# Performance work log

Measured on AMD Instinct MI355X. Metric: run time of the kernel, lower is better.

## Reference

```python
import jax, jax.numpy as jnp
import numpy as np

BIOSYNTHETIC_FAMILIES = {'glutamate': ['E','Q','P','R','K'], 'aspartate': ['D','N','T','I','M','K'], 'serine': ['S','G','C'], 'pyruvate': ['A','V','L'], 'aromatic': ['F','Y','W'], 'histidine': ['H']}
CODON_TABLE = {'UUU':'F','UUC':'F','UUA':'L','UUG':'L','CUU':'L','CUC':'L','CUA':'L','CUG':'L','AUU':'I','AUC':'I','AUA':'I','AUG':'M','GUU':'V','GUC':'V','GUA':'V','GUG':'V','UCU':'S','UCC':'S','UCA':'S','UCG':'S','CCU':'P','CCC':'P','CCA':'P','CCG':'P','ACU':'T','ACC':'T','ACA':'T','ACG':'T','GCU':'A','GCC':'A','GCA':'A','GCG':'A','UAU':'Y','UAC':'Y','UAA':'*','UAG':'*','CAU':'H','CAC':'H','CAA':'Q','CAG':'Q','AAU':'N','AAC':'N','AAA':'K','AAG':'K','GAU':'D','GAC':'D','GAA':'E','GAG':'E','UGU':'C','UGC':'C','UGA':'*','UGG':'W','CGU':'R','CGC':'R','CGA':'R','CGG':'R','AGU':'S','AGC':'S','AGA':'R','AGG':'R','GGU':'G','GGC':'G','GGA':'G','GGG':'G'}

def _build_family_matrix():
    aa2fam = {aa: f for f, aas in BIOSYNTHETIC_FAMILIES.items() for aa in aas}
    codons = list(CODON_TABLE.keys())
    fam = [aa2fam.get(CODON_TABLE[c]) for c in codons]  # None for stop codons
    M = np.zeros((64, 64), dtype=np.float32)
    for i in range(64):
        for j in range(64):
            if fam[i] is not None and fam[j] is not None and fam[i] == fam[j]:
                M[i, j] = 1.0
    return jnp.asarray(M)

FAMILY_MATRIX = _build_family_matrix()  # (64, 64) constant lookup table

def setup_inputs() -> dict:
    key = jax.random.key(0)
    k1, k2 = jax.random.split(key)
    codon_embeddings = jax.random.normal(k1, (16, 512, 16), dtype=jnp.float32)
    codon_indices = jax.random.randint(k2, (16, 512), 0, 64, dtype=jnp.int64 if jax.config.jax_enable_x64 else jnp.int32)
    return {"codon_embeddings": codon_embeddings, "codon_indices": codon_indices}

def reference(codon_embeddings, codon_indices):
    b, s, d = codon_embeddings.shape
    emb = codon_embeddings.reshape(-1, d)            # (n, d)
    idx = codon_indices.reshape(-1)                  # (n,)
    # Euclidean pairwise distances (torch.cdist, p=2)
    sq = jnp.sum(emb * emb, axis=-1)                 # (n,)
    d2 = sq[:, None] + sq[None, :] - 2.0 * (emb @ emb.T)
    d2 = jnp.maximum(d2, 0.0)
    mask = d2 > 0.0
    dist = jnp.where(mask, jnp.sqrt(jnp.where(mask, d2, 1.0)), 0.0)  # (n, n)
    # Same-family mask via 64x64 lookup gather
    same = FAMILY_MATRIX[idx[:, None], idx[None, :]]  # (n, n)
    eps = 1e-10
    same_sum = jnp.sum(same)
    total = jnp.asarray(dist.shape[0] * dist.shape[1], dist.dtype)
    same_d = jnp.sum(dist * same) / (same_sum + eps)
    diff_d = (jnp.sum(dist) - jnp.sum(dist * same)) / ((total - same_sum) + eps)
    loss = same_d - 0.5 * diff_d + 1.0
    return jax.nn.relu(loss)
```

## Files before the change

### kernel.cpp

```cpp
#include <hip/hip_runtime.h>
#include <math.h>

#define N_ROWS 8192
#define D 16
#define TILE 128
#define NT 64
#define NBLK 2080

#define OFF_PT   0
#define OFF_PS   16384
#define OFF_SQ   32768
#define OFF_FA   65536
#define OFF_FB   98304
#define OFF_EHI  131072
#define OFF_ELO  393216

typedef short  bf16x8 __attribute__((ext_vector_type(8)));
typedef float  f32x4  __attribute__((ext_vector_type(4)));

#if __has_builtin(__builtin_amdgcn_sqrtf)
#define SQRTF(x) __builtin_amdgcn_sqrtf(x)
#else
#define SQRTF(x) sqrtf(x)
#endif

__device__ __constant__ signed char FAM_LUT[64] = {
  4,4,3,3, 3,3,3,3,
  1,1,1,1, 3,3,3,3,
  2,2,2,2, 0,0,0,0,
  1,1,1,1, 3,3,3,3,
  4,4,-1,-1, 5,5,0,0,
  1,1,1,1, 1,1,0,0,
  2,2,-1,4, 0,0,0,0,
  2,2,0,0, 2,2,2,2
};

__device__ __forceinline__ unsigned short f2bf(float f) {
  unsigned u = __float_as_uint(f);
  u += 0x7fffu + ((u >> 16) & 1u);
  return (unsigned short)(u >> 16);
}
__device__ __forceinline__ float bf2f(unsigned short s) {
  return __uint_as_float((unsigned)s << 16);
}

__global__ __launch_bounds__(256) void prep_kernel(
    const float* __restrict__ emb, const int* __restrict__ idx,
    float* __restrict__ sq, float* __restrict__ fa, float* __restrict__ fb,
    unsigned short* __restrict__ ehi, unsigned short* __restrict__ elo) {
  const int i = blockIdx.x * 256 + threadIdx.x;
  const float4* src = (const float4*)(emb + (size_t)i * D);
  float v[16];
  float4 a0 = src[0], a1 = src[1], a2 = src[2], a3 = src[3];
  v[0]=a0.x; v[1]=a0.y; v[2]=a0.z; v[3]=a0.w;
  v[4]=a1.x; v[5]=a1.y; v[6]=a1.z; v[7]=a1.w;
  v[8]=a2.x; v[9]=a2.y; v[10]=a2.z; v[11]=a2.w;
  v[12]=a3.x; v[13]=a3.y; v[14]=a3.z; v[15]=a3.w;

  float s = v[0] * v[0];
  unsigned short hi[16], lo[16];
#pragma unroll
  for (int k = 0; k < 16; ++k) {
    if (k) s = fmaf(v[k], v[k], s);
    hi[k] = f2bf(v[k]);
    lo[k] = f2bf(v[k] - bf2f(hi[k]));
  }
  sq[i] = s;
  {
    bf16x8* dh = (bf16x8*)(ehi + (size_t)i * 16);
    bf16x8* dl = (bf16x8*)(elo + (size_t)i * 16);
    dh[0] = *(bf16x8*)&hi[0]; dh[1] = *(bf16x8*)&hi[8];
    dl[0] = *(bf16x8*)&lo[0]; dl[1] = *(bf16x8*)&lo[8];
  }
  const int f = FAM_LUT[idx[i] & 63];
  fa[i] = (f >= 0) ? (float)f : -1.0f;
  fb[i] = (f >= 0) ? (float)f : -2.0f;
}

__global__ __launch_bounds__(512, 4) void pair_kernel(
    const unsigned short* __restrict__ ehi, const unsigned short* __restrict__ elo,
    const float* __restrict__ sq,
    const float* __restrict__ fa, const float* __restrict__ fb,
    float* __restrict__ pt, float* __restrict__ ps) {
  const int u = blockIdx.y, bx = blockIdx.x;
  int it, jt;
  if (bx < NT - u) { it = u;          jt = u + bx; }
  else             { it = NT - 1 - u; jt = bx - 1; }

  __shared__ __align__(16) unsigned short BH[2048];
  __shared__ __align__(16) unsigned short BL[2048];
  __shared__ float2 SFJ[TILE];
  __shared__ float rT[8], rS[8];

  const int t  = threadIdx.x;
  const int w  = t >> 6;
  const int l  = t & 63;
  const int lr = l & 15;
  const int g  = l >> 4;
  const int half = g & 1;

  const unsigned short* asrc = (g < 2) ? ehi : elo;
  const int arow = it * TILE + w * 16 + lr;
  const bf16x8 afrag = *(const bf16x8*)(asrc + (size_t)arow * 16 + half * 8);
  float sqi[4], fai[4];
#pragma unroll
  for (int r = 0; r < 4; ++r) {
    const int irow = it * TILE + w * 16 + g * 4 + r;
    sqi[r] = sq[irow];
    fai[r] = fa[irow];
  }

  {
    const int c   = t & 255;
    const int mjs = c >> 5, hs = (c >> 4) & 1, lrs = c & 15;
    const int grow = jt * TILE + mjs * 16 + lrs;
    const unsigned short* src = (t < 256) ? ehi : elo;
    unsigned short*       dst = (t < 256) ? BH  : BL;
    *(bf16x8*)(dst + c * 8) = *(const bf16x8*)(src + (size_t)grow * 16 + hs * 8);
    if (t < TILE) SFJ[t] = make_float2(sq[jt * TILE + t], fb[jt * TILE + t]);
  }
  __syncthreads();

  const int bofs = (half * 16 + lr) * 8;
  float accT = 0.0f, accS = 0.0f;
#pragma unroll 2
  for (int mj = 0; mj < 8; ++mj) {
    const bf16x8 bhi = *(const bf16x8*)(BH + mj * 256 + bofs);
    const bf16x8 blo = *(const bf16x8*)(BL + mj * 256 + bofs);
    const float2 sfj = SFJ[mj * 16 + lr];
    f32x4 acc = {0.0f, 0.0f, 0.0f, 0.0f};
    acc = __builtin_amdgcn_mfma_f32_16x16x32_bf16(afrag, blo, acc, 0, 0, 0);
    acc = __builtin_amdgcn_mfma_f32_16x16x32_bf16(afrag, bhi, acc, 0, 0, 0);
#pragma unroll
    for (int r = 0; r < 4; ++r) {
      float d2 = fmaf(-2.0f, acc[r], sqi[r] + sfj.x);
      d2 = fmaxf(d2, 0.0f);
      const float dist = SQRTF(d2);
      accT += dist;
      accS += (fai[r] == sfj.y) ? dist : 0.0f;
    }
  }

#pragma unroll
  for (int off = 32; off > 0; off >>= 1) {
    accT += __shfl_down(accT, off);
    accS += __shfl_down(accS, off);
  }
  if (l == 0) { rT[w] = accT; rS[w] = accS; }
  __syncthreads();
  if (t == 0) {
    float sT = 0.0f, sS = 0.0f;
#pragma unroll
    for (int k = 0; k < 8; ++k) { sT += rT[k]; sS += rS[k]; }
    const float wgt = (it == jt) ? 1.0f : 2.0f;
    const int bid = blockIdx.y * gridDim.x + blockIdx.x;
    pt[bid] = wgt * sT;
    ps[bid] = wgt * sS;
  }
}

__global__ __launch_bounds__(1024) void final_kernel(
    const float* __restrict__ pt, const float* __restrict__ ps,
    const int* __restrict__ idx, float* __restrict__ out) {
  const int t = threadIdx.x;
  __shared__ int hist[8];
  __shared__ double rTd[16], rSd[16];
  if (t < 8) hist[t] = 0;
  __syncthreads();
  for (int k = t; k < N_ROWS; k += 1024) {
    const int f = FAM_LUT[idx[k] & 63];
    if (f >= 0) atomicAdd(&hist[f], 1);
  }

  double sT = 0.0, sS = 0.0;
  for (int k = t; k < NBLK; k += 1024) { sT += (double)pt[k]; sS += (double)ps[k]; }
#pragma unroll
  for (int off = 32; off > 0; off >>= 1) {
    sT += __shfl_down(sT, off);
    sS += __shfl_down(sS, off);
  }
  if ((t & 63) == 0) { rTd[t >> 6] = sT; rSd[t >> 6] = sS; }
  __syncthreads();
  if (t == 0) {
    double tot = 0.0, sam = 0.0;
#pragma unroll
    for (int k = 0; k < 16; ++k) { tot += rTd[k]; sam += rSd[k]; }
    double same_sum = 0.0;
    for (int f = 0; f < 6; ++f) { const double c = (double)hist[f]; same_sum += c * c; }
    const double total  = (double)N_ROWS * (double)N_ROWS;
    const double same_d = sam / (same_sum + 1e-10);
    const double diff_d = (tot - sam) / (total - same_sum + 1e-10);
    double loss = same_d - 0.5 * diff_d + 1.0;
    out[0] = (float)(loss > 0.0 ? loss : 0.0);
  }
}

extern "C" void kernel_launch(void* const* d_in, const int* in_sizes, int n_in,
                              void* d_out, int out_size, void* d_ws, size_t ws_size,
                              hipStream_t stream) {
  const float* emb = (const float*)d_in[0];
  const int*   idx = (const int*)d_in[1];
  char* ws = (char*)d_ws;
  float*          pt  = (float*)(ws + OFF_PT);
  float*          ps  = (float*)(ws + OFF_PS);
  float*          sqv = (float*)(ws + OFF_SQ);
  float*          fav = (float*)(ws + OFF_FA);
  float*          fbv = (float*)(ws + OFF_FB);
  unsigned short* ehi = (unsigned short*)(ws + OFF_EHI);
  unsigned short* elo = (unsigned short*)(ws + OFF_ELO);

  prep_kernel<<<dim3(N_ROWS / 256), dim3(256), 0, stream>>>(emb, idx, sqv, fav, fbv, ehi, elo);
  pair_kernel<<<dim3(NT + 1, NT / 2), dim3(512), 0, stream>>>(ehi, elo, sqv, fav, fbv, pt, ps);
  final_kernel<<<dim3(1), dim3(1024), 0, stream>>>(pt, ps, idx, (float*)d_out);
}
```

Measured before the change: 27.20 us.

## Fuse prep kernel into pair kernel and use ballot histogram in final

The separate prep kernel is removed. Each pair block now loads raw fp32 embeddings for its two tiles, computes squared norms, family codes and the bf16 hi/lo split on the fly into shared memory and registers. This drops one kernel launch and the workspace round trip, but every tile's rows are reconverted redundantly across many blocks. The final kernel also swaps its shared-memory atomic histogram for per-wave ballot/popcount counts and runs with 512 threads.

```diff
diff --git a/kernel.cpp b/kernel.cpp
--- a/kernel.cpp
+++ b/kernel.cpp
@@ -9,11 +9,6 @@
 
 #define OFF_PT   0
 #define OFF_PS   16384
-#define OFF_SQ   32768
-#define OFF_FA   65536
-#define OFF_FB   98304
-#define OFF_EHI  131072
-#define OFF_ELO  393216
 
 typedef short  bf16x8 __attribute__((ext_vector_type(8)));
 typedef float  f32x4  __attribute__((ext_vector_type(4)));
@@ -44,43 +39,8 @@
   return __uint_as_float((unsigned)s << 16);
 }
 
-__global__ __launch_bounds__(256) void prep_kernel(
+__global__ __launch_bounds__(512, 4) void pair_kernel(
     const float* __restrict__ emb, const int* __restrict__ idx,
-    float* __restrict__ sq, float* __restrict__ fa, float* __restrict__ fb,
-    unsigned short* __restrict__ ehi, unsigned short* __restrict__ elo) {
-  const int i = blockIdx.x * 256 + threadIdx.x;
-  const float4* src = (const float4*)(emb + (size_t)i * D);
-  float v[16];
-  float4 a0 = src[0], a1 = src[1], a2 = src[2], a3 = src[3];
-  v[0]=a0.x; v[1]=a0.y; v[2]=a0.z; v[3]=a0.w;
-  v[4]=a1.x; v[5]=a1.y; v[6]=a1.z; v[7]=a1.w;
-  v[8]=a2.x; v[9]=a2.y; v[10]=a2.z; v[11]=a2.w;
-  v[12]=a3.x; v[13]=a3.y; v[14]=a3.z; v[15]=a3.w;
-
-  float s = v[0] * v[0];
-  unsigned short hi[16], lo[16];
-#pragma unroll
-  for (int k = 0; k < 16; ++k) {
-    if (k) s = fmaf(v[k], v[k], s);
-    hi[k] = f2bf(v[k]);
-    lo[k] = f2bf(v[k] - bf2f(hi[k]));
-  }
-  sq[i] = s;
-  {
-    bf16x8* dh = (bf16x8*)(ehi + (size_t)i * 16);
-    bf16x8* dl = (bf16x8*)(elo + (size_t)i * 16);
-    dh[0] = *(bf16x8*)&hi[0]; dh[1] = *(bf16x8*)&hi[8];
-    dl[0] = *(bf16x8*)&lo[0]; dl[1] = *(bf16x8*)&lo[8];
-  }
-  const int f = FAM_LUT[idx[i] & 63];
-  fa[i] = (f >= 0) ? (float)f : -1.0f;
-  fb[i] = (f >= 0) ? (float)f : -2.0f;
-}
-
-__global__ __launch_bounds__(512, 4) void pair_kernel(
-    const unsigned short* __restrict__ ehi, const unsigned short* __restrict__ elo,
-    const float* __restrict__ sq,
-    const float* __restrict__ fa, const float* __restrict__ fb,
     float* __restrict__ pt, float* __restrict__ ps) {
   const int u = blockIdx.y, bx = blockIdx.x;
   int it, jt;
@@ -90,7 +50,9 @@
   __shared__ __align__(16) unsigned short BH[2048];
   __shared__ __align__(16) unsigned short BL[2048];
   __shared__ float2 SFJ[TILE];
-  __shared__ float rT[8], rS[8];
+  __shared__ float  SQI[TILE];
+  __shared__ float  FAI[TILE];
+  __shared__ float  rT[8], rS[8];
 
   const int t  = threadIdx.x;
   const int w  = t >> 6;
@@ -99,27 +61,64 @@
   const int g  = l >> 4;
   const int half = g & 1;
 
-  const unsigned short* asrc = (g < 2) ? ehi : elo;
+  if (t < 256) {
+    const int local = t & 127;
+    const int row = ((t < 128) ? it : jt) * TILE + local;
+    const float4* s4 = (const float4*)(emb + (size_t)row * D);
+    float4 a0 = s4[0], a1 = s4[1], a2 = s4[2], a3 = s4[3];
+    float v[16];
+    v[0]=a0.x; v[1]=a0.y; v[2]=a0.z; v[3]=a0.w;
+    v[4]=a1.x; v[5]=a1.y; v[6]=a1.z; v[7]=a1.w;
+    v[8]=a2.x; v[9]=a2.y; v[10]=a2.z; v[11]=a2.w;
+    v[12]=a3.x; v[13]=a3.y; v[14]=a3.z; v[15]=a3.w;
+    float ss = v[0] * v[0];
+#pragma unroll
+    for (int k = 1; k < 16; ++k) ss = fmaf(v[k], v[k], ss);
+    const int f = FAM_LUT[idx[row] & 63];
+    if (t < 128) { SQI[local] = ss; FAI[local] = (f >= 0) ? (float)f : -1.0f; }
+    else         { SFJ[local] = make_float2(ss, (f >= 0) ? (float)f : -2.0f); }
+  }
+
+  if (t < 256) {
+    const int mjs = t >> 5, hs = (t >> 4) & 1, lrs = t & 15;
+    const int row = jt * TILE + mjs * 16 + lrs;
+    const float4* s4 = (const float4*)(emb + (size_t)row * D + hs * 8);
+    float4 b0 = s4[0], b1 = s4[1];
+    float vb[8];
+    vb[0]=b0.x; vb[1]=b0.y; vb[2]=b0.z; vb[3]=b0.w;
+    vb[4]=b1.x; vb[5]=b1.y; vb[6]=b1.z; vb[7]=b1.w;
+    unsigned short h8[8], l8[8];
+#pragma unroll
+    for (int k = 0; k < 8; ++k) {
+      h8[k] = f2bf(vb[k]);
+      l8[k] = f2bf(vb[k] - bf2f(h8[k]));
+    }
+    *(bf16x8*)(BH + t * 8) = *(bf16x8*)h8;
+    *(bf16x8*)(BL + t * 8) = *(bf16x8*)l8;
+  }
+
   const int arow = it * TILE + w * 16 + lr;
-  const bf16x8 afrag = *(const bf16x8*)(asrc + (size_t)arow * 16 + half * 8);
+  const float4* a4 = (const float4*)(emb + (size_t)arow * D + half * 8);
+  float4 c0 = a4[0], c1 = a4[1];
+  float va[8];
+  va[0]=c0.x; va[1]=c0.y; va[2]=c0.z; va[3]=c0.w;
+  va[4]=c1.x; va[5]=c1.y; va[6]=c1.z; va[7]=c1.w;
+  unsigned short f8[8];
+#pragma unroll
+  for (int k = 0; k < 8; ++k) {
+    const unsigned short h = f2bf(va[k]);
+    f8[k] = (g < 2) ? h : f2bf(va[k] - bf2f(h));
+  }
+  const bf16x8 afrag = *(bf16x8*)f8;
+
+  __syncthreads();
+
   float sqi[4], fai[4];
 #pragma unroll
   for (int r = 0; r < 4; ++r) {
-    const int irow = it * TILE + w * 16 + g * 4 + r;
-    sqi[r] = sq[irow];
-    fai[r] = fa[irow];
-  }
-
-  {
-    const int c   = t & 255;
-    const int mjs = c >> 5, hs = (c >> 4) & 1, lrs = c & 15;
-    const int grow = jt * TILE + mjs * 16 + lrs;
-    const unsigned short* src = (t < 256) ? ehi : elo;
-    unsigned short*       dst = (t < 256) ? BH  : BL;
-    *(bf16x8*)(dst + c * 8) = *(const bf16x8*)(src + (size_t)grow * 16 + hs * 8);
-    if (t < TILE) SFJ[t] = make_float2(sq[jt * TILE + t], fb[jt * TILE + t]);
-  }
-  __syncthreads();
+    sqi[r] = SQI[w * 16 + g * 4 + r];
+    fai[r] = FAI[w * 16 + g * 4 + r];
+  }
 
   const int bofs = (half * 16 + lr) * 8;
   float accT = 0.0f, accS = 0.0f;
@@ -159,34 +158,44 @@
   }
 }
 
-__global__ __launch_bounds__(1024) void final_kernel(
+__global__ __launch_bounds__(512) void final_kernel(
     const float* __restrict__ pt, const float* __restrict__ ps,
     const int* __restrict__ idx, float* __restrict__ out) {
-  const int t = threadIdx.x;
-  __shared__ int hist[8];
-  __shared__ double rTd[16], rSd[16];
-  if (t < 8) hist[t] = 0;
-  __syncthreads();
-  for (int k = t; k < N_ROWS; k += 1024) {
-    const int f = FAM_LUT[idx[k] & 63];
-    if (f >= 0) atomicAdd(&hist[f], 1);
-  }
+  const int t = threadIdx.x, w = t >> 6, l = t & 63;
+  __shared__ float  HW[8][8];
+  __shared__ double rTd[8], rSd[8];
+
+  float myCnt = 0.0f;
+#pragma unroll
+  for (int rr = 0; rr < 16; ++rr) {
+    const int f = FAM_LUT[idx[rr * 512 + t] & 63];
+#pragma unroll
+    for (int fam = 0; fam < 6; ++fam) {
+      const unsigned long long m = __ballot(f == fam);
+      if (l == fam) myCnt += (float)__popcll(m);
+    }
+  }
+  if (l < 8) HW[w][l] = (l < 6) ? myCnt : 0.0f;
 
   double sT = 0.0, sS = 0.0;
-  for (int k = t; k < NBLK; k += 1024) { sT += (double)pt[k]; sS += (double)ps[k]; }
+  for (int k = t; k < NBLK; k += 512) { sT += (double)pt[k]; sS += (double)ps[k]; }
 #pragma unroll
   for (int off = 32; off > 0; off >>= 1) {
     sT += __shfl_down(sT, off);
     sS += __shfl_down(sS, off);
   }
-  if ((t & 63) == 0) { rTd[t >> 6] = sT; rSd[t >> 6] = sS; }
+  if (l == 0) { rTd[w] = sT; rSd[w] = sS; }
   __syncthreads();
   if (t == 0) {
     double tot = 0.0, sam = 0.0;
 #pragma unroll
-    for (int k = 0; k < 16; ++k) { tot += rTd[k]; sam += rSd[k]; }
+    for (int k = 0; k < 8; ++k) { tot += rTd[k]; sam += rSd[k]; }
     double same_sum = 0.0;
-    for (int f = 0; f < 6; ++f) { const double c = (double)hist[f]; same_sum += c * c; }
+    for (int f = 0; f < 6; ++f) {
+      double c = 0.0;
+      for (int k = 0; k < 8; ++k) c += (double)HW[k][f];
+      same_sum += c * c;
+    }
     const double total  = (double)N_ROWS * (double)N_ROWS;
     const double same_d = sam / (same_sum + 1e-10);
     const double diff_d = (tot - sam) / (total - same_sum + 1e-10);
@@ -201,15 +210,9 @@
   const float* emb = (const float*)d_in[0];
   const int*   idx = (const int*)d_in[1];
   char* ws = (char*)d_ws;
-  float*          pt  = (float*)(ws + OFF_PT);
-  float*          ps  = (float*)(ws + OFF_PS);
-  float*          sqv = (float*)(ws + OFF_SQ);
-  float*          fav = (float*)(ws + OFF_FA);
-  float*          fbv = (float*)(ws + OFF_FB);
-  unsigned short* ehi = (unsigned short*)(ws + OFF_EHI);
-  unsigned short* elo = (unsigned short*)(ws + OFF_ELO);
-
-  prep_kernel<<<dim3(N_ROWS / 256), dim3(256), 0, stream>>>(emb, idx, sqv, fav, fbv, ehi, elo);
-  pair_kernel<<<dim3(NT + 1, NT / 2), dim3(512), 0, stream>>>(ehi, elo, sqv, fav, fbv, pt, ps);
-  final_kernel<<<dim3(1), dim3(1024), 0, stream>>>(pt, ps, idx, (float*)d_out);
-}
+  float* pt = (float*)(ws + OFF_PT);
+  float* ps = (float*)(ws + OFF_PS);
+
+  pair_kernel<<<dim3(NT + 1, NT / 2), dim3(512), 0, stream>>>(emb, idx, pt, ps);
+  final_kernel<<<dim3(1), dim3(512), 0, stream>>>(pt, ps, idx, (float*)d_out);
+}
```

Result: no change. 27.02 us (-0.6%).

## Fold squared norms and family mask into augmented bf16 MFMA operands

Applied to the files above, without the earlier changes.

Packs the -2·x hi/lo split, the squared norms, and constant ones into 32-wide augmented bf16 vectors, so the MFMA accumulator directly yields the full squared distance. The same-family test becomes a third MFMA over one-hot family vectors, which replaces per-element compares and scalar loads. The final kernel's family histogram now uses wave ballots instead of shared atomics. In exchange it issues a third MFMA per tile and reads more data per row, and it changes the precision structure of the d2 computation (sq carried as a bf16 hi/lo pair, some lo terms dropped).

```diff
diff --git a/kernel.cpp b/kernel.cpp
--- a/kernel.cpp
+++ b/kernel.cpp
@@ -7,13 +7,12 @@
 #define NT 64
 #define NBLK 2080
 
-#define OFF_PT   0
-#define OFF_PS   16384
-#define OFF_SQ   32768
-#define OFF_FA   65536
-#define OFF_FB   98304
-#define OFF_EHI  131072
-#define OFF_ELO  393216
+#define OFF_PT    0
+#define OFF_PS    16384
+#define OFF_AP    32768
+#define OFF_B1    557056
+#define OFF_B2    1081344
+#define OFF_FOH   1605632
 
 typedef short  bf16x8 __attribute__((ext_vector_type(8)));
 typedef float  f32x4  __attribute__((ext_vector_type(4)));
@@ -46,8 +45,8 @@
 
 __global__ __launch_bounds__(256) void prep_kernel(
     const float* __restrict__ emb, const int* __restrict__ idx,
-    float* __restrict__ sq, float* __restrict__ fa, float* __restrict__ fb,
-    unsigned short* __restrict__ ehi, unsigned short* __restrict__ elo) {
+    unsigned short* __restrict__ aP, unsigned short* __restrict__ b1,
+    unsigned short* __restrict__ b2, unsigned short* __restrict__ foh) {
   const int i = blockIdx.x * 256 + threadIdx.x;
   const float4* src = (const float4*)(emb + (size_t)i * D);
   float v[16];
@@ -57,39 +56,58 @@
   v[8]=a2.x; v[9]=a2.y; v[10]=a2.z; v[11]=a2.w;
   v[12]=a3.x; v[13]=a3.y; v[14]=a3.z; v[15]=a3.w;
 
-  float s = v[0] * v[0];
-  unsigned short hi[16], lo[16];
+  float sq = v[0] * v[0];
+#pragma unroll
+  for (int k = 1; k < 16; ++k) sq = fmaf(v[k], v[k], sq);
+  const unsigned short sqh = f2bf(sq);
+  const unsigned short sql = f2bf(sq - bf2f(sqh));
+  const unsigned short ONE = 0x3F80;
+
+  unsigned short ah[16], al[16], bh[16], bl[16];
 #pragma unroll
   for (int k = 0; k < 16; ++k) {
-    if (k) s = fmaf(v[k], v[k], s);
-    hi[k] = f2bf(v[k]);
-    lo[k] = f2bf(v[k] - bf2f(hi[k]));
-  }
-  sq[i] = s;
-  {
-    bf16x8* dh = (bf16x8*)(ehi + (size_t)i * 16);
-    bf16x8* dl = (bf16x8*)(elo + (size_t)i * 16);
-    dh[0] = *(bf16x8*)&hi[0]; dh[1] = *(bf16x8*)&hi[8];
-    dl[0] = *(bf16x8*)&lo[0]; dl[1] = *(bf16x8*)&lo[8];
+    bh[k] = f2bf(v[k]);
+    bl[k] = f2bf(v[k] - bf2f(bh[k]));
+    const float s = -2.0f * v[k];
+    ah[k] = f2bf(s);
+    al[k] = f2bf(s - bf2f(ah[k]));
+  }
+
+  unsigned short A[32], B1[32], B2[32];
+#pragma unroll
+  for (int k = 0; k < 16; ++k) { A[k] = ah[k]; B1[k] = bh[k]; B2[k] = bl[k]; }
+#pragma unroll
+  for (int k = 0; k < 12; ++k) { A[16+k] = al[k]; B1[16+k] = bh[k]; B2[16+k] = bl[k]; }
+  A[28] = ONE;  A[29] = sqh;  A[30] = sql;  A[31] = al[15];
+  B1[28] = sqh; B1[29] = ONE; B1[30] = ONE; B1[31] = bh[15];
+  B2[28] = sql; B2[29] = 0;   B2[30] = 0;   B2[31] = bl[15];
+
+#pragma unroll
+  for (int c = 0; c < 4; ++c) {
+    *(bf16x8*)(aP + (size_t)i * 32 + c * 8) = *(bf16x8*)&A[c * 8];
+    *(bf16x8*)(b1 + (size_t)i * 32 + c * 8) = *(bf16x8*)&B1[c * 8];
+    *(bf16x8*)(b2 + (size_t)i * 32 + c * 8) = *(bf16x8*)&B2[c * 8];
   }
   const int f = FAM_LUT[idx[i] & 63];
-  fa[i] = (f >= 0) ? (float)f : -1.0f;
-  fb[i] = (f >= 0) ? (float)f : -2.0f;
+  unsigned short oh[8];
+#pragma unroll
+  for (int k = 0; k < 8; ++k) oh[k] = (f == k) ? ONE : (unsigned short)0;
+  *(bf16x8*)(foh + (size_t)i * 8) = *(bf16x8*)oh;
 }
 
 __global__ __launch_bounds__(512, 4) void pair_kernel(
-    const unsigned short* __restrict__ ehi, const unsigned short* __restrict__ elo,
-    const float* __restrict__ sq,
-    const float* __restrict__ fa, const float* __restrict__ fb,
+    const unsigned short* __restrict__ aP, const unsigned short* __restrict__ b1g,
+    const unsigned short* __restrict__ b2g, const unsigned short* __restrict__ fohg,
     float* __restrict__ pt, float* __restrict__ ps) {
   const int u = blockIdx.y, bx = blockIdx.x;
   int it, jt;
   if (bx < NT - u) { it = u;          jt = u + bx; }
   else             { it = NT - 1 - u; jt = bx - 1; }
 
-  __shared__ __align__(16) unsigned short BH[2048];
-  __shared__ __align__(16) unsigned short BL[2048];
-  __shared__ float2 SFJ[TILE];
+  __shared__ __align__(16) unsigned short LB1[4096];
+  __shared__ __align__(16) unsigned short LB2[4096];
+  __shared__ __align__(16) unsigned short LFB[1024];
+  __shared__ __align__(16) unsigned short LZ[8];
   __shared__ float rT[8], rS[8];
 
   const int t  = threadIdx.x;
@@ -97,47 +115,44 @@
   const int l  = t & 63;
   const int lr = l & 15;
   const int g  = l >> 4;
-  const int half = g & 1;
-
-  const unsigned short* asrc = (g < 2) ? ehi : elo;
+
+  {
+    const int rl = t >> 2, c = t & 3;
+    const size_t gb = (size_t)(jt * TILE + rl) * 32 + c * 8;
+    *(bf16x8*)(LB1 + rl * 32 + c * 8) = *(const bf16x8*)(b1g + gb);
+    *(bf16x8*)(LB2 + rl * 32 + c * 8) = *(const bf16x8*)(b2g + gb);
+    if (t < TILE) *(bf16x8*)(LFB + t * 8) =
+        *(const bf16x8*)(fohg + (size_t)(jt * TILE + t) * 8);
+    if (t == 128) { bf16x8 z = {0,0,0,0,0,0,0,0}; *(bf16x8*)LZ = z; }
+  }
+
   const int arow = it * TILE + w * 16 + lr;
-  const bf16x8 afrag = *(const bf16x8*)(asrc + (size_t)arow * 16 + half * 8);
-  float sqi[4], fai[4];
-#pragma unroll
-  for (int r = 0; r < 4; ++r) {
-    const int irow = it * TILE + w * 16 + g * 4 + r;
-    sqi[r] = sq[irow];
-    fai[r] = fa[irow];
-  }
-
-  {
-    const int c   = t & 255;
-    const int mjs = c >> 5, hs = (c >> 4) & 1, lrs = c & 15;
-    const int grow = jt * TILE + mjs * 16 + lrs;
-    const unsigned short* src = (t < 256) ? ehi : elo;
-    unsigned short*       dst = (t < 256) ? BH  : BL;
-    *(bf16x8*)(dst + c * 8) = *(const bf16x8*)(src + (size_t)grow * 16 + hs * 8);
-    if (t < TILE) SFJ[t] = make_float2(sq[jt * TILE + t], fb[jt * TILE + t]);
-  }
+  const bf16x8 afrag = *(const bf16x8*)(aP + (size_t)arow * 32 + g * 8);
+  bf16x8 afrag3;
+  if (g == 0) afrag3 = *(const bf16x8*)(fohg + (size_t)arow * 8);
+  else        { bf16x8 z = {0,0,0,0,0,0,0,0}; afrag3 = z; }
+
   __syncthreads();
 
-  const int bofs = (half * 16 + lr) * 8;
+  const unsigned short* p3 = (g == 0) ? (LFB + lr * 8) : LZ;
+  const int step3 = (g == 0) ? 128 : 0;
+  const int boff  = lr * 32 + g * 8;
+  const f32x4 zf = {0.0f, 0.0f, 0.0f, 0.0f};
   float accT = 0.0f, accS = 0.0f;
 #pragma unroll 2
   for (int mj = 0; mj < 8; ++mj) {
-    const bf16x8 bhi = *(const bf16x8*)(BH + mj * 256 + bofs);
-    const bf16x8 blo = *(const bf16x8*)(BL + mj * 256 + bofs);
-    const float2 sfj = SFJ[mj * 16 + lr];
-    f32x4 acc = {0.0f, 0.0f, 0.0f, 0.0f};
-    acc = __builtin_amdgcn_mfma_f32_16x16x32_bf16(afrag, blo, acc, 0, 0, 0);
-    acc = __builtin_amdgcn_mfma_f32_16x16x32_bf16(afrag, bhi, acc, 0, 0, 0);
+    const bf16x8 f1 = *(const bf16x8*)(LB1 + mj * 512 + boff);
+    const bf16x8 f2 = *(const bf16x8*)(LB2 + mj * 512 + boff);
+    const bf16x8 f3 = *(const bf16x8*)(p3 + mj * step3);
+    f32x4 acc = __builtin_amdgcn_mfma_f32_16x16x32_bf16(afrag, f1, zf, 0, 0, 0);
+    acc = __builtin_amdgcn_mfma_f32_16x16x32_bf16(afrag, f2, acc, 0, 0, 0);
+    const f32x4 msk = __builtin_amdgcn_mfma_f32_16x16x32_bf16(afrag3, f3, zf, 0, 0, 0);
 #pragma unroll
     for (int r = 0; r < 4; ++r) {
-      float d2 = fmaf(-2.0f, acc[r], sqi[r] + sfj.x);
-      d2 = fmaxf(d2, 0.0f);
+      const float d2   = fmaxf(acc[r], 0.0f);
       const float dist = SQRTF(d2);
       accT += dist;
-      accS += (fai[r] == sfj.y) ? dist : 0.0f;
+      accS = fmaf(msk[r], dist, accS);
     }
   }
 
@@ -162,15 +177,24 @@
 __global__ __launch_bounds__(1024) void final_kernel(
     const float* __restrict__ pt, const float* __restrict__ ps,
     const int* __restrict__ idx, float* __restrict__ out) {
-  const int t = threadIdx.x;
-  __shared__ int hist[8];
+  const int t = threadIdx.x, w = t >> 6, l = t & 63;
+  __shared__ float  HW[16][8];
   __shared__ double rTd[16], rSd[16];
-  if (t < 8) hist[t] = 0;
-  __syncthreads();
-  for (int k = t; k < N_ROWS; k += 1024) {
-    const int f = FAM_LUT[idx[k] & 63];
-    if (f >= 0) atomicAdd(&hist[f], 1);
-  }
+
+  const int4* p4 = (const int4*)idx;
+  const int4 va = p4[t], vb = p4[t + 1024];
+  int vals[8] = {va.x, va.y, va.z, va.w, vb.x, vb.y, vb.z, vb.w};
+  float myCnt = 0.0f;
+#pragma unroll
+  for (int rr = 0; rr < 8; ++rr) {
+    const int f = FAM_LUT[vals[rr] & 63];
+#pragma unroll
+    for (int fam = 0; fam < 6; ++fam) {
+      const unsigned long long mk = __ballot(f == fam);
+      if (l == fam) myCnt += (float)__popcll(mk);
+    }
+  }
+  if (l < 8) HW[w][l] = (l < 6) ? myCnt : 0.0f;
 
   double sT = 0.0, sS = 0.0;
   for (int k = t; k < NBLK; k += 1024) { sT += (double)pt[k]; sS += (double)ps[k]; }
@@ -179,14 +203,18 @@
     sT += __shfl_down(sT, off);
     sS += __shfl_down(sS, off);
   }
-  if ((t & 63) == 0) { rTd[t >> 6] = sT; rSd[t >> 6] = sS; }
+  if (l == 0) { rTd[w] = sT; rSd[w] = sS; }
   __syncthreads();
   if (t == 0) {
     double tot = 0.0, sam = 0.0;
 #pragma unroll
     for (int k = 0; k < 16; ++k) { tot += rTd[k]; sam += rSd[k]; }
     double same_sum = 0.0;
-    for (int f = 0; f < 6; ++f) { const double c = (double)hist[f]; same_sum += c * c; }
+    for (int f = 0; f < 6; ++f) {
+      double c = 0.0;
+      for (int k = 0; k < 16; ++k) c += (double)HW[k][f];
+      same_sum += c * c;
+    }
     const double total  = (double)N_ROWS * (double)N_ROWS;
     const double same_d = sam / (same_sum + 1e-10);
     const double diff_d = (tot - sam) / (total - same_sum + 1e-10);
@@ -203,13 +231,12 @@
   char* ws = (char*)d_ws;
   float*          pt  = (float*)(ws + OFF_PT);
   float*          ps  = (float*)(ws + OFF_PS);
-  float*          sqv = (float*)(ws + OFF_SQ);
-  float*          fav = (float*)(ws + OFF_FA);
-  float*          fbv = (float*)(ws + OFF_FB);
-  unsigned short* ehi = (unsigned short*)(ws + OFF_EHI);
-  unsigned short* elo = (unsigned short*)(ws + OFF_ELO);
-
-  prep_kernel<<<dim3(N_ROWS / 256), dim3(256), 0, stream>>>(emb, idx, sqv, fav, fbv, ehi, elo);
-  pair_kernel<<<dim3(NT + 1, NT / 2), dim3(512), 0, stream>>>(ehi, elo, sqv, fav, fbv, pt, ps);
+  unsigned short* aP  = (unsigned short*)(ws + OFF_AP);
+  unsigned short* b1  = (unsigned short*)(ws + OFF_B1);
+  unsigned short* b2  = (unsigned short*)(ws + OFF_B2);
+  unsigned short* foh = (unsigned short*)(ws + OFF_FOH);
+
+  prep_kernel<<<dim3(N_ROWS / 256), dim3(256), 0, stream>>>(emb, idx, aP, b1, b2, foh);
+  pair_kernel<<<dim3(NT + 1, NT / 2), dim3(512), 0, stream>>>(aP, b1, b2, foh, pt, ps);
   final_kernel<<<dim3(1), dim3(1024), 0, stream>>>(pt, ps, idx, (float*)d_out);
 }
```

Measured after the change: 26.40 us. -2.9%, faster.
